# Optimization experiments

Hardware: AMD Instinct MI355X
Metric: run time of the kernel (lower is better)

## Reference

```python
import jax, jax.numpy as jnp
import numpy as np

D_K = 64
SCALE = 1.0 / (D_K ** 0.5)
NEG_INF = float('-inf')


def setup_inputs() -> dict:
    key = jax.random.key(0)
    kq, kk, kv = jax.random.split(key, 3)
    B, H, S, D = 2, 16, 2048, D_K
    Q = jax.random.normal(kq, (B, H, S, D), dtype=jnp.float32)
    K = jax.random.normal(kk, (B, H, S, D), dtype=jnp.float32)
    V = jax.random.normal(kv, (B, H, S, D), dtype=jnp.float32)
    # causal mask: True = attend, False = masked (matches masked_fill(mask == False, -inf))
    mask = jnp.tril(jnp.ones((S, S), dtype=jnp.bool_))
    return {"Q": Q, "K": K, "V": V, "mask": mask}


def reference(Q, K, V, mask):
    # scores: [B, H, q, k]
    scores = jnp.einsum('bhqd,bhkd->bhqk', Q, K) * SCALE
    scores = jnp.where(mask, scores, NEG_INF)
    # hand-rolled stable softmax, same math as the torch module
    x_exp = jnp.exp(scores - jnp.max(scores, axis=-1, keepdims=True))
    attn = x_exp / jnp.sum(x_exp, axis=-1, keepdims=True)
    out = jnp.einsum('bhqk,bhkv->bhqv', attn, V)
    return out
```

## Files before the change

kernel.cpp:

```cpp
#include <hip/hip_runtime.h>
#include <hip/hip_bf16.h>

#define S_LEN   2048
#define D_DIM   64
#define BK      64
#define NBH     32

typedef __attribute__((ext_vector_type(8))) short  short8;
typedef __attribute__((ext_vector_type(4))) float  floatx4;

#define KLD   72
#define VTLD  72
#define PLD   72
#define OLD   65

#define VOFF  9216
#define POFF  18432
#define SMEM_BYTES 36864

__device__ __forceinline__ unsigned pk2(float lo, float hi) {
  __hip_bfloat162 h = __float22bfloat162_rn(float2{lo, hi});
  union { __hip_bfloat162 v; unsigned u; } c; c.v = h;
  return c.u;
}
__device__ __forceinline__ short8 pk8(const float* f) {
  union { short8 s; unsigned u[4]; } r;
  r.u[0] = pk2(f[0], f[1]); r.u[1] = pk2(f[2], f[3]);
  r.u[2] = pk2(f[4], f[5]); r.u[3] = pk2(f[6], f[7]);
  return r.s;
}
__device__ __forceinline__ float bf2f(unsigned short s) {
  union { unsigned u; float f; } c; c.u = ((unsigned)s) << 16; return c.f;
}

__global__ __launch_bounds__(256, 2)
void prep(const float* __restrict__ K, const float* __restrict__ V,
          unsigned short* __restrict__ Kbf, unsigned short* __restrict__ Vt)
{
  __shared__ unsigned short vt[64 * KLD];
  const int tid = threadIdx.x;
  const int bh  = blockIdx.x >> 5;
  const int k0  = (blockIdx.x & 31) * 64;

  {
    const int k   = k0 + (tid >> 2);
    const int seg = (tid & 3) * 16;
    const float* p = K + ((size_t)(bh * S_LEN + k)) * D_DIM + seg;
    union { float4 v[4]; float f[16]; } u;
    u.v[0] = *(const float4*)p;       u.v[1] = *(const float4*)(p + 4);
    u.v[2] = *(const float4*)(p + 8); u.v[3] = *(const float4*)(p + 12);
    unsigned short* dst = Kbf + ((size_t)(bh * S_LEN + k)) * D_DIM + seg;
    *(short8*)dst       = pk8(u.f);
    *(short8*)(dst + 8) = pk8(u.f + 8);
  }
  {
    const int kp2 = tid & 31;
    const int dg  = (tid >> 5) * 8;
    const float* p = V + ((size_t)(bh * S_LEN + k0 + 2 * kp2)) * D_DIM + dg;
    union { float4 v[2]; float f[8]; } x, y;
    x.v[0] = *(const float4*)p;            x.v[1] = *(const float4*)(p + 4);
    y.v[0] = *(const float4*)(p + D_DIM);  y.v[1] = *(const float4*)(p + D_DIM + 4);
#pragma unroll
    for (int i = 0; i < 8; ++i)
      *(unsigned*)&vt[(dg + i) * KLD + 2 * kp2] = pk2(x.f[i], y.f[i]);
  }
  __syncthreads();
  {
    const int d   = tid >> 2;
    const int seg = (tid & 3) * 16;
    short8 a = *(short8*)&vt[d * KLD + seg];
    short8 b = *(short8*)&vt[d * KLD + seg + 8];
    unsigned short* dst = Vt + ((size_t)(bh * D_DIM + d)) * S_LEN + k0 + seg;
    *(short8*)dst       = a;
    *(short8*)(dst + 8) = b;
  }
}

__global__ __launch_bounds__(256, 2)
void fa_fwd(const float* __restrict__ Qg,
            const unsigned short* __restrict__ Kbf,
            const unsigned short* __restrict__ Vt,
            float* __restrict__ Og,
            unsigned short* __restrict__ Opart,
            float* __restrict__ Lpart)
{
  __shared__ char smem[SMEM_BYTES];
  short* Klds  = (short*)smem;
  short* Vtlds = (short*)(smem + VOFF);

  const int tid  = threadIdx.x;
  const int wv   = tid >> 6;
  const int lane = tid & 63;
  const int col  = lane & 15;
  const int quad = lane >> 4;
  short* PA = (short*)(smem + POFF) + wv * (32 * PLD);
  short* PB = PA + 16 * PLD;
  float* Olds = (float*)smem + wv * (16 * OLD);

  int qi, bh, it0, itend, half = 0;
  bool split;
  if (blockIdx.x < 512) {
    split = true;
    qi    = 15 - ((int)blockIdx.x >> 6);
    bh    = ((int)blockIdx.x >> 1) & 31;
    half  = blockIdx.x & 1;
    const int nk = 2 * (qi + 1);
    const int h0 = nk >> 1;
    it0   = half ? h0 : 0;
    itend = half ? nk : h0;
  } else {
    split = false;
    const int u = blockIdx.x - 512;
    qi    = 7 - (u >> 5);
    bh    = u & 31;
    it0   = 0;
    itend = 2 * (qi + 1);
  }
  const int q0 = qi * 128;

  const float qscale = 0.18033688011112042f;
  const float*          Qb  = Qg  + (size_t)bh * S_LEN * D_DIM;
  const unsigned short* Kb  = Kbf + (size_t)bh * S_LEN * D_DIM;
  const unsigned short* Vtb = Vt  + (size_t)bh * D_DIM * S_LEN;
  float*                Ob  = Og  + (size_t)bh * S_LEN * D_DIM;

  const int srow = tid >> 2;
  const int sseg = (tid & 3) * 16;

  const int qws[2] = {q0 + wv * 16, q0 + 64 + wv * 16};

  short8 qf[2][2];
#pragma unroll
  for (int qt = 0; qt < 2; ++qt)
#pragma unroll
    for (int h = 0; h < 2; ++h) {
      const float* qp = Qb + (size_t)(qws[qt] + col) * D_DIM + h * 32 + quad * 8;
      union { float4 v[2]; float f[8]; } u;
      u.v[0] = *(const float4*)qp; u.v[1] = *(const float4*)(qp + 4);
      float t[8];
#pragma unroll
      for (int j = 0; j < 8; ++j) t[j] = u.f[j] * qscale;
      qf[qt][h] = pk8(t);
    }

  floatx4 o[2][4];
#pragma unroll
  for (int qt = 0; qt < 2; ++qt)
#pragma unroll
    for (int dt = 0; dt < 4; ++dt) o[qt][dt] = (floatx4){0.f,0.f,0.f,0.f};
  float l_run[2] = {0.f, 0.f};

  short8 kpre[2], vpre[2];
  {
    const unsigned short* kp = Kb  + (size_t)(it0 * BK + srow) * D_DIM + sseg;
    kpre[0] = *(const short8*)kp;  kpre[1] = *(const short8*)(kp + 8);
    const unsigned short* vp = Vtb + (size_t)srow * S_LEN + it0 * BK + sseg;
    vpre[0] = *(const short8*)vp;  vpre[1] = *(const short8*)(vp + 8);
  }

  for (int it = it0; it < itend; ++it) {
    __syncthreads();
    *(short8*)&Klds [srow * KLD  + sseg]     = kpre[0];
    *(short8*)&Klds [srow * KLD  + sseg + 8] = kpre[1];
    *(short8*)&Vtlds[srow * VTLD + sseg]     = vpre[0];
    *(short8*)&Vtlds[srow * VTLD + sseg + 8] = vpre[1];
    __syncthreads();

    if (it + 1 < itend) {
      const int kb2 = (it + 1) * BK;
      const unsigned short* kp = Kb  + (size_t)(kb2 + srow) * D_DIM + sseg;
      kpre[0] = *(const short8*)kp;  kpre[1] = *(const short8*)(kp + 8);
      const unsigned short* vp = Vtb + (size_t)srow * S_LEN + kb2 + sseg;
      vpre[0] = *(const short8*)vp;  vpre[1] = *(const short8*)(vp + 8);
    }

    const int  kb  = it * BK;
    const bool doA = (kb != q0 + 64);

    floatx4 st[2][4];
#pragma unroll
    for (int kt = 0; kt < 4; ++kt) {
      short8 kf0 = *(short8*)&Klds[(kt * 16 + col) * KLD + quad * 8];
      short8 kf1 = *(short8*)&Klds[(kt * 16 + col) * KLD + 32 + quad * 8];
      floatx4 c = (floatx4){0.f,0.f,0.f,0.f};
      c = __builtin_amdgcn_mfma_f32_16x16x32_bf16(kf0, qf[1][0], c, 0, 0, 0);
      c = __builtin_amdgcn_mfma_f32_16x16x32_bf16(kf1, qf[1][1], c, 0, 0, 0);
      st[1][kt] = c;
      if (doA) {
        floatx4 d = (floatx4){0.f,0.f,0.f,0.f};
        d = __builtin_amdgcn_mfma_f32_16x16x32_bf16(kf0, qf[0][0], d, 0, 0, 0);
        d = __builtin_amdgcn_mfma_f32_16x16x32_bf16(kf1, qf[0][1], d, 0, 0, 0);
        st[0][kt] = d;
      }
    }

    if (kb == q0) {
      const int qg = qws[0] + col;
#pragma unroll
      for (int kt = 0; kt < 4; ++kt)
#pragma unroll
        for (int r = 0; r < 4; ++r)
          if (kb + kt * 16 + quad * 4 + r > qg) st[0][kt][r] = -3.0e38f;
    }
    if (!doA) {
      const int qg = qws[1] + col;
#pragma unroll
      for (int kt = 0; kt < 4; ++kt)
#pragma unroll
        for (int r = 0; r < 4; ++r)
          if (kb + kt * 16 + quad * 4 + r > qg) st[1][kt][r] = -3.0e38f;
    }

#pragma unroll
    for (int qt = 0; qt < 2; ++qt) {
      if (qt == 0 && !doA) continue;
      float lsum = 0.f;
#pragma unroll
      for (int kt = 0; kt < 4; ++kt)
#pragma unroll
        for (int r = 0; r < 4; ++r) {
          const float p = __builtin_amdgcn_exp2f(st[qt][kt][r]);
          st[qt][kt][r] = p;
          lsum += p;
        }
      l_run[qt] += lsum;
      short* Pq = qt ? PB : PA;
#pragma unroll
      for (int kt = 0; kt < 4; ++kt) {
        uint2 w; w.x = pk2(st[qt][kt][0], st[qt][kt][1]); w.y = pk2(st[qt][kt][2], st[qt][kt][3]);
        *(uint2*)&Pq[col * PLD + kt * 16 + quad * 4] = w;
      }
    }

#pragma unroll
    for (int g = 0; g < 2; ++g) {
      short8 pfB = *(short8*)&PB[col * PLD + g * 32 + quad * 8];
      short8 pfA;
      if (doA) pfA = *(short8*)&PA[col * PLD + g * 32 + quad * 8];
#pragma unroll
      for (int dt = 0; dt < 4; ++dt) {
        short8 vf = *(short8*)&Vtlds[(dt * 16 + col) * VTLD + g * 32 + quad * 8];
        o[1][dt] = __builtin_amdgcn_mfma_f32_16x16x32_bf16(vf, pfB, o[1][dt], 0, 0, 0);
        if (doA)
          o[0][dt] = __builtin_amdgcn_mfma_f32_16x16x32_bf16(vf, pfA, o[0][dt], 0, 0, 0);
      }
    }
  }

  __syncthreads();
#pragma unroll
  for (int qt = 0; qt < 2; ++qt) {
    float l = l_run[qt];
    l += __shfl_xor(l, 16);
    l += __shfl_xor(l, 32);
    if (!split) {
      const float inv = 1.0f / l;
#pragma unroll
      for (int dt = 0; dt < 4; ++dt)
#pragma unroll
        for (int r = 0; r < 4; ++r)
          Olds[col * OLD + dt * 16 + quad * 4 + r] = o[qt][dt][r] * inv;
#pragma unroll
      for (int it2 = 0; it2 < 4; ++it2) {
        const int ql = it2 * 4 + quad;
        float4 w;
        w.x = Olds[ql * OLD + col * 4 + 0];
        w.y = Olds[ql * OLD + col * 4 + 1];
        w.z = Olds[ql * OLD + col * 4 + 2];
        w.w = Olds[ql * OLD + col * 4 + 3];
        *(float4*)(Ob + (size_t)(qws[qt] + ql) * D_DIM + col * 4) = w;
      }
    } else {
#pragma unroll
      for (int dt = 0; dt < 4; ++dt)
#pragma unroll
        for (int r = 0; r < 4; ++r)
          Olds[col * OLD + dt * 16 + quad * 4 + r] = o[qt][dt][r];
#pragma unroll
      for (int it2 = 0; it2 < 4; ++it2) {
        const int ql = it2 * 4 + quad;
        const int p  = qws[qt] + ql - 1024;
        float4 w;
        w.x = Olds[ql * OLD + col * 4 + 0];
        w.y = Olds[ql * OLD + col * 4 + 1];
        w.z = Olds[ql * OLD + col * 4 + 2];
        w.w = Olds[ql * OLD + col * 4 + 3];
        uint2 pw; pw.x = pk2(w.x, w.y); pw.y = pk2(w.z, w.w);
        *(uint2*)&Opart[((size_t)(half * 32 + bh) * 1024 + p) * 64 + col * 4] = pw;
      }
      if (quad == 0)
        Lpart[(half * 32 + bh) * 1024 + (qws[qt] + col - 1024)] = l;
    }
  }
}

__global__ __launch_bounds__(256, 2)
void merge(const unsigned short* __restrict__ Opart,
           const float* __restrict__ Lpart,
           float* __restrict__ Og)
{
  const int tid = threadIdx.x;
  const int gid = blockIdx.x * 64 + (tid >> 2);
  const int seg = (tid & 3) * 16;
  const int bh  = gid >> 10;
  const int p   = gid & 1023;
  const float la = Lpart[(0 * 32 + bh) * 1024 + p];
  const float lb = Lpart[(1 * 32 + bh) * 1024 + p];
  const float inv = 1.0f / (la + lb);
  const unsigned short* pa = Opart + ((size_t)(0 * 32 + bh) * 1024 + p) * 64 + seg;
  const unsigned short* pb = Opart + ((size_t)(1 * 32 + bh) * 1024 + p) * 64 + seg;
  union { short8 s; unsigned short h[8]; } a0, a1, b0, b1;
  a0.s = *(short8*)pa; a1.s = *(short8*)(pa + 8);
  b0.s = *(short8*)pb; b1.s = *(short8*)(pb + 8);
  float out[16];
#pragma unroll
  for (int j = 0; j < 8; ++j) out[j]     = (bf2f(a0.h[j]) + bf2f(b0.h[j])) * inv;
#pragma unroll
  for (int j = 0; j < 8; ++j) out[8 + j] = (bf2f(a1.h[j]) + bf2f(b1.h[j])) * inv;
  float* dst = Og + ((size_t)bh * S_LEN + 1024 + p) * D_DIM + seg;
#pragma unroll
  for (int j = 0; j < 4; ++j)
    *(float4*)(dst + 4 * j) = *(float4*)&out[4 * j];
}

extern "C" void kernel_launch(void* const* d_in, const int* in_sizes, int n_in,
                              void* d_out, int out_size, void* d_ws, size_t ws_size,
                              hipStream_t stream) {
  const float* Q = (const float*)d_in[0];
  const float* K = (const float*)d_in[1];
  const float* V = (const float*)d_in[2];
  float* O = (float*)d_out;
  unsigned short* Kbf   = (unsigned short*)d_ws;
  unsigned short* Vt    = Kbf + (size_t)NBH * S_LEN * D_DIM;
  unsigned short* Opart = Vt  + (size_t)NBH * S_LEN * D_DIM;
  float*          Lpart = (float*)(Opart + (size_t)2 * 32 * 1024 * 64);

  hipLaunchKernelGGL(prep,   dim3(NBH * (S_LEN / 64)), dim3(256), 0, stream, K, V, Kbf, Vt);
  hipLaunchKernelGGL(fa_fwd, dim3(768), dim3(256), 0, stream, Q, Kbf, Vt, O, Opart, Lpart);
  hipLaunchKernelGGL(merge,  dim3(512), dim3(256), 0, stream, Opart, Lpart, O);
}
```

Measured before the change: 141.4 us.

## Split causal attention into fixed 8-tile KV chunks and load K/V fragments directly

Replaces the two-way split of the upper query tiles with a table-driven schedule that cuts each query tile's KV range into chunks of at most 8 tiles, giving 1280 more uniform blocks. The merge kernel is generalised to sum up to four partials per row. K and V MFMA fragments are now loaded straight from global memory into registers instead of being staged through LDS, which removes the per-iteration barriers and the register prefetch. In exchange, the loads are less coalesced and no longer overlap with compute, and more partial outputs must be written and merged.

```diff
diff --git a/kernel.cpp b/kernel.cpp
--- a/kernel.cpp
+++ b/kernel.cpp
@@ -10,13 +10,14 @@
 typedef __attribute__((ext_vector_type(4))) float  floatx4;
 
 #define KLD   72
-#define VTLD  72
 #define PLD   72
 #define OLD   65
-
-#define VOFF  9216
-#define POFF  18432
-#define SMEM_BYTES 36864
+#define SMEM_BYTES 18432
+
+__constant__ int c_slot_qi[40] = {15,15,15,15,14,14,14,13,13,13,12,12,12,11,11,11,10,10,9,9,8,8,7,7,6,5,4,3, 14,10,6,2, 13,9,5,1, 12,8,4,0};
+__constant__ int c_slot_p [40] = { 0, 1, 2, 3, 0, 1, 2, 0, 1, 2, 0, 1, 2, 0, 1, 2, 0, 1,0,1,0,1,0,1,0,0,0,0,  3, 2,1,0,  3,2,1,0,  3,2,1,0};
+__constant__ int c_pfx[16] = {0,1,2,3,4,6,8,10,12,15,18,21,24,28,32,36};
+__constant__ int c_np [16] = {1,1,1,1,2,2,2,2,3,3,3,3,4,4,4,4};
 
 __device__ __forceinline__ unsigned pk2(float lo, float hi) {
   __hip_bfloat162 h = __float22bfloat162_rn(float2{lo, hi});
@@ -85,37 +86,24 @@
             float* __restrict__ Lpart)
 {
   __shared__ char smem[SMEM_BYTES];
-  short* Klds  = (short*)smem;
-  short* Vtlds = (short*)(smem + VOFF);
 
   const int tid  = threadIdx.x;
   const int wv   = tid >> 6;
   const int lane = tid & 63;
   const int col  = lane & 15;
   const int quad = lane >> 4;
-  short* PA = (short*)(smem + POFF) + wv * (32 * PLD);
+  short* PA = (short*)smem + wv * (32 * PLD);
   short* PB = PA + 16 * PLD;
-  float* Olds = (float*)smem + wv * (16 * OLD);
-
-  int qi, bh, it0, itend, half = 0;
-  bool split;
-  if (blockIdx.x < 512) {
-    split = true;
-    qi    = 15 - ((int)blockIdx.x >> 6);
-    bh    = ((int)blockIdx.x >> 1) & 31;
-    half  = blockIdx.x & 1;
-    const int nk = 2 * (qi + 1);
-    const int h0 = nk >> 1;
-    it0   = half ? h0 : 0;
-    itend = half ? nk : h0;
-  } else {
-    split = false;
-    const int u = blockIdx.x - 512;
-    qi    = 7 - (u >> 5);
-    bh    = u & 31;
-    it0   = 0;
-    itend = 2 * (qi + 1);
-  }
+  float* Olds = (float*)PA;
+
+  const int slot = blockIdx.x >> 5;
+  const int bh   = blockIdx.x & 31;
+  const int qi   = c_slot_qi[slot];
+  const int part = c_slot_p[slot];
+  const int nk   = 2 * (qi + 1);
+  const int it0  = part * 8;
+  const int itend = (it0 + 8 < nk) ? it0 + 8 : nk;
+  const bool multi = (c_np[qi] > 1);
   const int q0 = qi * 128;
 
   const float qscale = 0.18033688011112042f;
@@ -124,9 +112,6 @@
   const unsigned short* Vtb = Vt  + (size_t)bh * D_DIM * S_LEN;
   float*                Ob  = Og  + (size_t)bh * S_LEN * D_DIM;
 
-  const int srow = tid >> 2;
-  const int sseg = (tid & 3) * 16;
-
   const int qws[2] = {q0 + wv * 16, q0 + 64 + wv * 16};
 
   short8 qf[2][2];
@@ -150,49 +135,39 @@
     for (int dt = 0; dt < 4; ++dt) o[qt][dt] = (floatx4){0.f,0.f,0.f,0.f};
   float l_run[2] = {0.f, 0.f};
 
-  short8 kpre[2], vpre[2];
-  {
-    const unsigned short* kp = Kb  + (size_t)(it0 * BK + srow) * D_DIM + sseg;
-    kpre[0] = *(const short8*)kp;  kpre[1] = *(const short8*)(kp + 8);
-    const unsigned short* vp = Vtb + (size_t)srow * S_LEN + it0 * BK + sseg;
-    vpre[0] = *(const short8*)vp;  vpre[1] = *(const short8*)(vp + 8);
-  }
-
   for (int it = it0; it < itend; ++it) {
-    __syncthreads();
-    *(short8*)&Klds [srow * KLD  + sseg]     = kpre[0];
-    *(short8*)&Klds [srow * KLD  + sseg + 8] = kpre[1];
-    *(short8*)&Vtlds[srow * VTLD + sseg]     = vpre[0];
-    *(short8*)&Vtlds[srow * VTLD + sseg + 8] = vpre[1];
-    __syncthreads();
-
-    if (it + 1 < itend) {
-      const int kb2 = (it + 1) * BK;
-      const unsigned short* kp = Kb  + (size_t)(kb2 + srow) * D_DIM + sseg;
-      kpre[0] = *(const short8*)kp;  kpre[1] = *(const short8*)(kp + 8);
-      const unsigned short* vp = Vtb + (size_t)srow * S_LEN + kb2 + sseg;
-      vpre[0] = *(const short8*)vp;  vpre[1] = *(const short8*)(vp + 8);
-    }
-
     const int  kb  = it * BK;
     const bool doA = (kb != q0 + 64);
 
+    short8 kfr[4][2];
+#pragma unroll
+    for (int kt = 0; kt < 4; ++kt) {
+      const unsigned short* kp = Kb + (size_t)(kb + kt * 16 + col) * D_DIM + quad * 8;
+      kfr[kt][0] = *(const short8*)kp;
+      kfr[kt][1] = *(const short8*)(kp + 32);
+    }
+
     floatx4 st[2][4];
 #pragma unroll
     for (int kt = 0; kt < 4; ++kt) {
-      short8 kf0 = *(short8*)&Klds[(kt * 16 + col) * KLD + quad * 8];
-      short8 kf1 = *(short8*)&Klds[(kt * 16 + col) * KLD + 32 + quad * 8];
       floatx4 c = (floatx4){0.f,0.f,0.f,0.f};
-      c = __builtin_amdgcn_mfma_f32_16x16x32_bf16(kf0, qf[1][0], c, 0, 0, 0);
-      c = __builtin_amdgcn_mfma_f32_16x16x32_bf16(kf1, qf[1][1], c, 0, 0, 0);
+      c = __builtin_amdgcn_mfma_f32_16x16x32_bf16(kfr[kt][0], qf[1][0], c, 0, 0, 0);
+      c = __builtin_amdgcn_mfma_f32_16x16x32_bf16(kfr[kt][1], qf[1][1], c, 0, 0, 0);
       st[1][kt] = c;
       if (doA) {
         floatx4 d = (floatx4){0.f,0.f,0.f,0.f};
-        d = __builtin_amdgcn_mfma_f32_16x16x32_bf16(kf0, qf[0][0], d, 0, 0, 0);
-        d = __builtin_amdgcn_mfma_f32_16x16x32_bf16(kf1, qf[0][1], d, 0, 0, 0);
+        d = __builtin_amdgcn_mfma_f32_16x16x32_bf16(kfr[kt][0], qf[0][0], d, 0, 0, 0);
+        d = __builtin_amdgcn_mfma_f32_16x16x32_bf16(kfr[kt][1], qf[0][1], d, 0, 0, 0);
         st[0][kt] = d;
       }
     }
+
+    short8 vfr[2][4];
+#pragma unroll
+    for (int g = 0; g < 2; ++g)
+#pragma unroll
+      for (int dt = 0; dt < 4; ++dt)
+        vfr[g][dt] = *(const short8*)(Vtb + (size_t)(dt * 16 + col) * S_LEN + kb + g * 32 + quad * 8);
 
     if (kb == q0) {
       const int qg = qws[0] + col;
@@ -239,21 +214,19 @@
       if (doA) pfA = *(short8*)&PA[col * PLD + g * 32 + quad * 8];
 #pragma unroll
       for (int dt = 0; dt < 4; ++dt) {
-        short8 vf = *(short8*)&Vtlds[(dt * 16 + col) * VTLD + g * 32 + quad * 8];
-        o[1][dt] = __builtin_amdgcn_mfma_f32_16x16x32_bf16(vf, pfB, o[1][dt], 0, 0, 0);
+        o[1][dt] = __builtin_amdgcn_mfma_f32_16x16x32_bf16(vfr[g][dt], pfB, o[1][dt], 0, 0, 0);
         if (doA)
-          o[0][dt] = __builtin_amdgcn_mfma_f32_16x16x32_bf16(vf, pfA, o[0][dt], 0, 0, 0);
-      }
-    }
-  }
-
-  __syncthreads();
+          o[0][dt] = __builtin_amdgcn_mfma_f32_16x16x32_bf16(vfr[g][dt], pfA, o[0][dt], 0, 0, 0);
+      }
+    }
+  }
+
 #pragma unroll
   for (int qt = 0; qt < 2; ++qt) {
     float l = l_run[qt];
     l += __shfl_xor(l, 16);
     l += __shfl_xor(l, 32);
-    if (!split) {
+    if (!multi) {
       const float inv = 1.0f / l;
 #pragma unroll
       for (int dt = 0; dt < 4; ++dt)
@@ -276,20 +249,21 @@
 #pragma unroll
         for (int r = 0; r < 4; ++r)
           Olds[col * OLD + dt * 16 + quad * 4 + r] = o[qt][dt][r];
+      const size_t prow = (size_t)bh * 5120 + (size_t)(c_pfx[qi] + part) * 128;
 #pragma unroll
       for (int it2 = 0; it2 < 4; ++it2) {
         const int ql = it2 * 4 + quad;
-        const int p  = qws[qt] + ql - 1024;
+        const int qlocal = qt * 64 + wv * 16 + ql;
         float4 w;
         w.x = Olds[ql * OLD + col * 4 + 0];
         w.y = Olds[ql * OLD + col * 4 + 1];
         w.z = Olds[ql * OLD + col * 4 + 2];
         w.w = Olds[ql * OLD + col * 4 + 3];
         uint2 pw; pw.x = pk2(w.x, w.y); pw.y = pk2(w.z, w.w);
-        *(uint2*)&Opart[((size_t)(half * 32 + bh) * 1024 + p) * 64 + col * 4] = pw;
+        *(uint2*)&Opart[(prow + qlocal) * 64 + col * 4] = pw;
       }
       if (quad == 0)
-        Lpart[(half * 32 + bh) * 1024 + (qws[qt] + col - 1024)] = l;
+        Lpart[prow + qt * 64 + wv * 16 + col] = l;
     }
   }
 }
@@ -302,25 +276,35 @@
   const int tid = threadIdx.x;
   const int gid = blockIdx.x * 64 + (tid >> 2);
   const int seg = (tid & 3) * 16;
-  const int bh  = gid >> 10;
-  const int p   = gid & 1023;
-  const float la = Lpart[(0 * 32 + bh) * 1024 + p];
-  const float lb = Lpart[(1 * 32 + bh) * 1024 + p];
-  const float inv = 1.0f / (la + lb);
-  const unsigned short* pa = Opart + ((size_t)(0 * 32 + bh) * 1024 + p) * 64 + seg;
-  const unsigned short* pb = Opart + ((size_t)(1 * 32 + bh) * 1024 + p) * 64 + seg;
-  union { short8 s; unsigned short h[8]; } a0, a1, b0, b1;
-  a0.s = *(short8*)pa; a1.s = *(short8*)(pa + 8);
-  b0.s = *(short8*)pb; b1.s = *(short8*)(pb + 8);
-  float out[16];
-#pragma unroll
-  for (int j = 0; j < 8; ++j) out[j]     = (bf2f(a0.h[j]) + bf2f(b0.h[j])) * inv;
-#pragma unroll
-  for (int j = 0; j < 8; ++j) out[8 + j] = (bf2f(a1.h[j]) + bf2f(b1.h[j])) * inv;
-  float* dst = Og + ((size_t)bh * S_LEN + 1024 + p) * D_DIM + seg;
+  const int bh  = gid / 1536;
+  const int rem = gid - bh * 1536;
+  const int qi  = 4 + (rem >> 7);
+  const int ql  = rem & 127;
+  const int np  = c_np[qi];
+  const size_t base = (size_t)bh * 5120 + (size_t)c_pfx[qi] * 128 + ql;
+
+  float acc[16];
+#pragma unroll
+  for (int j = 0; j < 16; ++j) acc[j] = 0.f;
+  float l = 0.f;
+  for (int p = 0; p < np; ++p) {
+    const size_t row = base + (size_t)p * 128;
+    l += Lpart[row];
+    const unsigned short* pp = Opart + row * 64 + seg;
+    union { short8 s; unsigned short h[8]; } a0, a1;
+    a0.s = *(short8*)pp; a1.s = *(short8*)(pp + 8);
+#pragma unroll
+    for (int j = 0; j < 8; ++j) acc[j]     += bf2f(a0.h[j]);
+#pragma unroll
+    for (int j = 0; j < 8; ++j) acc[8 + j] += bf2f(a1.h[j]);
+  }
+  const float inv = 1.0f / l;
+  float* dst = Og + ((size_t)bh * S_LEN + qi * 128 + ql) * D_DIM + seg;
+#pragma unroll
+  for (int j = 0; j < 16; ++j) acc[j] *= inv;
 #pragma unroll
   for (int j = 0; j < 4; ++j)
-    *(float4*)(dst + 4 * j) = *(float4*)&out[4 * j];
+    *(float4*)(dst + 4 * j) = *(float4*)&acc[4 * j];
 }
 
 extern "C" void kernel_launch(void* const* d_in, const int* in_sizes, int n_in,
@@ -333,9 +317,9 @@
   unsigned short* Kbf   = (unsigned short*)d_ws;
   unsigned short* Vt    = Kbf + (size_t)NBH * S_LEN * D_DIM;
   unsigned short* Opart = Vt  + (size_t)NBH * S_LEN * D_DIM;
-  float*          Lpart = (float*)(Opart + (size_t)2 * 32 * 1024 * 64);
+  float*          Lpart = (float*)(Opart + (size_t)NBH * 5120 * 64);
 
   hipLaunchKernelGGL(prep,   dim3(NBH * (S_LEN / 64)), dim3(256), 0, stream, K, V, Kbf, Vt);
-  hipLaunchKernelGGL(fa_fwd, dim3(768), dim3(256), 0, stream, Q, Kbf, Vt, O, Opart, Lpart);
-  hipLaunchKernelGGL(merge,  dim3(512), dim3(256), 0, stream, Opart, Lpart, O);
-}
+  hipLaunchKernelGGL(fa_fwd, dim3(40 * NBH), dim3(256), 0, stream, Q, Kbf, Vt, O, Opart, Lpart);
+  hipLaunchKernelGGL(merge,  dim3(768), dim3(256), 0, stream, Opart, Lpart, O);
+}
```

Result: slower. 180.9 us (+27.9%).
